# Optimization experiments

Measured on AMD Instinct MI355X. Metric: run time of the kernel, lower is better.

Reference implementation:

```python
import jax, jax.numpy as jnp
import numpy as np

B, T, DIM = 1, 2048, 2048
H, KV, D = 16, 4, 128
REP = H // KV
L, S = 32, 16          # cmp_len, cmp_stride
LP = 64                # slc_block
TOPK = 16
WIN = 512
CMP_HID = 2 * D
GATE_HID = DIM // 4
SCALE = D ** -0.5
TC = (T - L) // S + 1  # number of compressed blocks
NS = T // LP           # number of selection blocks
NEG = -1e30


def setup_inputs() -> dict:
    key = jax.random.key(0)
    ks = jax.random.split(key, 12)
    n = lambda k, sh: jax.random.normal(k, sh, jnp.float32) * 0.02
    return dict(
        x=jax.random.normal(ks[0], (B, T, DIM), jnp.float32),
        W_qkv=n(ks[1], ((H + 2 * KV) * D, DIM)), b_qkv=jnp.zeros(((H + 2 * KV) * D,), jnp.float32),
        W_out=n(ks[2], (DIM, H * D)), b_out=jnp.zeros((DIM,), jnp.float32),
        sinks=jnp.zeros((H,), jnp.float32),
        cmp_pos=n(ks[3], (L, D)),
        W_c1=n(ks[4], (CMP_HID, L * D)), b_c1=jnp.zeros((CMP_HID,), jnp.float32),
        W_c2=n(ks[5], (D, CMP_HID)), b_c2=jnp.zeros((D,), jnp.float32),
        W_g1=n(ks[6], (GATE_HID, DIM)), b_g1=jnp.zeros((GATE_HID,), jnp.float32),
        W_g2=n(ks[7], (3, GATE_HID)), b_g2=jnp.array([-2.2, -2.2, 1.4], jnp.float32),
    )


def _nsa(x, W_qkv, b_qkv, W_out, b_out, sinks, cmp_pos,
         W_c1, b_c1, W_c2, b_c2, W_g1, b_g1, W_g2, b_g2):
    qkv = x @ W_qkv.T + b_qkv
    q = qkv[..., :H * D].reshape(B, T, H, D)
    k = qkv[..., H * D:(H + KV) * D].reshape(B, T, KV, D)
    v = qkv[..., (H + KV) * D:].reshape(B, T, KV, D)

    t_idx = jnp.arange(T)
    # ---- compression phi over overlapping blocks (Eq 7) ----
    starts = jnp.arange(TC) * S
    gidx = starts[:, None] + jnp.arange(L)[None, :]          # [TC,L]

    def compress(z):                                          # [B,T,KV,D] -> [B,TC,KV,D]
        blk = z[:, gidx] + cmp_pos[None, None, :, None, :]    # [B,TC,L,KV,D]
        blk = blk.transpose(0, 1, 3, 2, 4).reshape(B, TC, KV, L * D)
        h = jax.nn.gelu(blk @ W_c1.T + b_c1, approximate=False)
        return h @ W_c2.T + b_c2

    k_cmp = jnp.repeat(compress(k), REP, axis=2)              # [B,TC,H,D]
    v_cmp = jnp.repeat(compress(v), REP, axis=2)

    # ---- CMP attention (Eq 8) ----
    c_logits = jnp.einsum('bthd,bchd->bhtc', q, k_cmp) * SCALE
    valid = (starts[None, :] + L - 1) <= t_idx[:, None]       # block fully in past [T,TC]
    c_logits = jnp.where(valid[None, None], c_logits, NEG)
    p = jax.nn.softmax(c_logits, axis=-1)
    any_valid = valid.any(axis=-1)                            # [T]
    p = jnp.where(any_valid[None, None, :, None], p, 0.0)
    o_cmp = jnp.einsum('bhtc,bchd->bthd', p, v_cmp)

    # ---- block score aggregation (Eq 9) + head sum (Eq 10) ----
    j_idx = jnp.arange(NS)
    ov = (starts[None, :] < (j_idx[:, None] + 1) * LP) & (starts[None, :] + L > j_idx[:, None] * LP)
    blk_scores = jnp.einsum('bhtc,jc->btj', p, ov.astype(p.dtype))  # [B,T,NS]
    cur_blk = t_idx // LP
    masked = jnp.where((j_idx[None, :] >= cur_blk[:, None])[None], -jnp.inf, blk_scores)
    _, dyn_idx = jax.lax.top_k(masked, TOPK - 3)              # Eq 11 (3 fixed blocks)
    fixed = jnp.stack([jnp.zeros_like(cur_blk), jnp.clip(cur_blk - 2, 0),
                       jnp.clip(cur_blk - 1, 0)], axis=-1)    # [T,3]
    all_blk = jnp.concatenate([jnp.broadcast_to(fixed[None], (B, T, 3)), dyn_idx], axis=-1)

    # ---- SLC sparse block attention (Eq 12) ----
    allowed = jax.nn.one_hot(all_blk, NS).sum(-2) > 0         # [B,T,NS]
    allowed = allowed | (j_idx[None, None, :] == cur_blk[None, :, None])  # own block dense
    tok_allowed = jnp.repeat(allowed, LP, axis=-1)            # [B,T,T]
    causal = t_idx[None, :] <= t_idx[:, None]                 # [T,T] (query, key)
    K = jnp.repeat(k, REP, axis=2)
    V = jnp.repeat(v, REP, axis=2)
    base = jnp.einsum('bthd,bshd->bhts', q, K) * SCALE        # shared logits
    s_logits = jnp.where((tok_allowed & causal[None])[:, None], base, NEG)
    o_slc = jnp.einsum('bhts,bshd->bthd', jax.nn.softmax(s_logits, -1), V)

    # ---- SWA sliding window with attention sinks ----
    swa_mask = causal & (t_idx[None, :] > t_idx[:, None] - WIN)
    w_logits = jnp.where(swa_mask[None, None], base, NEG)
    sink = jnp.broadcast_to(sinks[None, :, None, None], (B, H, T, 1))
    pw = jax.nn.softmax(jnp.concatenate([w_logits, sink], axis=-1), -1)[..., :T]
    o_swa = jnp.einsum('bhts,bshd->bthd', pw, V)

    # ---- sigmoid gating (Eq 5) + output proj ----
    g = jax.nn.sigmoid(jax.nn.gelu(x @ W_g1.T + b_g1, approximate=False) @ W_g2.T + b_g2)
    o = (g[..., 0, None, None] * o_cmp + g[..., 1, None, None] * o_slc
         + g[..., 2, None, None] * o_swa)                     # [B,T,H,D]
    return o.reshape(B, T, H * D) @ W_out.T + b_out


def reference(x, W_qkv, b_qkv, W_out, b_out, sinks, cmp_pos,
              W_c1, b_c1, W_c2, b_c2, W_g1, b_g1, W_g2, b_g2):
    return _nsa(x, W_qkv, b_qkv, W_out, b_out, sinks, cmp_pos,
                W_c1, b_c1, W_c2, b_c2, W_g1, b_g1, W_g2, b_g2)
```

## Files before the change

kernel.cpp:

```cpp
#include <hip/hip_runtime.h>
#include <hip/hip_bf16.h>

#define DEV static __device__ __forceinline__

constexpr int T_ = 2048, DIM_ = 2048, H_ = 16, KVH = 4, D_ = 128;
constexpr int LL = 32, SS = 16, TOPK_ = 16, WIN_ = 512;
constexpr int GATE_HID_ = 512;
constexpr int TC_ = 127, NS_ = 32;
constexpr int QKV_N = (H_ + 2 * KVH) * D_;
constexpr float SCALE_ = 0.08838834764831845f;

typedef __attribute__((ext_vector_type(8))) short short8;
typedef __attribute__((ext_vector_type(4))) float f32x4;
typedef __attribute__((ext_vector_type(4))) float float4v;
typedef __attribute__((ext_vector_type(4))) unsigned short u16x4;

DEV unsigned short f2b(float x) {
    return __builtin_bit_cast(unsigned short, __float2bfloat16(x));
}
DEV float b2f(unsigned short u) { return __builtin_bit_cast(float, ((unsigned)u) << 16); }
DEV float gelu_f(float x) { return 0.5f * x * (1.f + erff(x * 0.70710678118654752f)); }

DEV void g2l16(const void* g, void* l) {
    __builtin_amdgcn_global_load_lds((const __attribute__((address_space(1))) unsigned int*)g,
// ... 12 lines not shown

__global__ void cvt_all(const float* __restrict__ x, const float* __restrict__ wq,
                        const float* __restrict__ wg, const float* __restrict__ wc1,
                        const float* __restrict__ wc2,
                        unsigned short* __restrict__ xb, unsigned short* __restrict__ wqb,
                        unsigned short* __restrict__ wgb, unsigned short* __restrict__ wc1b,
                        unsigned short* __restrict__ wc2b) {
    const long i = ((long)blockIdx.x * 256 + threadIdx.x) * 4;
    const float* s;
    unsigned short* d;
    long off;
    if (i < 4194304)        { s = x;   d = xb;   off = i; }
    else if (i < 10485760)  { s = wq;  d = wqb;  off = i - 4194304; }
    else if (i < 11534336)  { s = wg;  d = wgb;  off = i - 10485760; }
    else if (i < 12582912)  { s = wc1; d = wc1b; off = i - 11534336; }
    else if (i < 12615680)  { s = wc2; d = wc2b; off = i - 12582912; }
    else return;
    float4v v = *(const float4v*)(s + off);
    u16x4 o;
#pragma unroll
    for (int j = 0; j < 4; j++) o[j] = f2b(v[j]);
    *(u16x4*)(d + off) = o;
}

DEV void stage64(const unsigned short* __restrict__ src, unsigned short* dstL,
                 int K, int tid) {
#pragma unroll
    for (int it = 0; it < 4; it++) {
        const int e = it * 256 + tid;
        const int row = e >> 3, cg = e & 7;
        g2l16(src + (size_t)row * K + ((cg ^ (row & 7)) << 3), dstL + e * 8);
    }
}
DEV short8 frag64(const unsigned short* Ls, int row, int g) {
    return *(const short8*)&Ls[row * 64 + ((g ^ (row & 7)) << 3)];
}

template <int ACT, bool WF, bool WB>
__global__ __launch_bounds__(256) void gemm_f(const unsigned short* __restrict__ A,
                                              const unsigned short* __restrict__ B,
                                              const float* __restrict__ bias,
                                              float* __restrict__ Cf,
                                              unsigned short* __restrict__ Cb,
                                              int M, int N, int K) {
    __shared__ __align__(16) unsigned short As[128 * 64];
    __shared__ __align__(16) unsigned short Bs[128 * 64];
    const int tid = threadIdx.x;
    const int w = tid >> 6, l = tid & 63;
    const int lc = l & 15, lg = l >> 4;
    const int wr = w >> 1, wc = w & 1;
    const int m0 = blockIdx.y * 128, n0 = blockIdx.x * 128;
    f32x4 acc[4][4] = {};
    for (int k0 = 0; k0 < K; k0 += 64) {
        stage64(A + (size_t)m0 * K + k0, As, K, tid);
        stage64(B + (size_t)n0 * K + k0, Bs, K, tid);
        __syncthreads();
#pragma unroll
        for (int ks = 0; ks < 2; ks++) {
            short8 af[4], bfr[4];
#pragma unroll
            for (int mi = 0; mi < 4; mi++) af[mi] = frag64(As, wr * 64 + mi * 16 + lc, ks * 4 + lg);
#pragma unroll
            for (int ni = 0; ni < 4; ni++) bfr[ni] = frag64(Bs, wc * 64 + ni * 16 + lc, ks * 4 + lg);
#pragma unroll
            for (int mi = 0; mi < 4; mi++)
#pragma unroll
                for (int ni = 0; ni < 4; ni++)
                    acc[mi][ni] = __builtin_amdgcn_mfma_f32_16x16x32_bf16(af[mi], bfr[ni], acc[mi][ni], 0, 0, 0);
        }
        __syncthreads();
    }
#pragma unroll
    for (int mi = 0; mi < 4; mi++) {
        const int gr = m0 + wr * 64 + mi * 16 + lg * 4;
#pragma unroll
        for (int ni = 0; ni < 4; ni++) {
            const int gc = n0 + wc * 64 + ni * 16 + lc;
            const float bv = bias[gc];
#pragma unroll
            for (int r = 0; r < 4; r++) {
                float v = acc[mi][ni][r] + bv;
                if (ACT == 1) v = gelu_f(v);
                const size_t idx = (size_t)(gr + r) * N + gc;
                if (WF) Cf[idx] = v;
                if (WB) Cb[idx] = f2b(v);
            }
        }
    }
}

__global__ __launch_bounds__(256) void gemm_qkvg(const unsigned short* __restrict__ A,
                                                 const unsigned short* __restrict__ Bq,
                                                 const unsigned short* __restrict__ Bg,
                                                 const float* __restrict__ bq,
                                                 const float* __restrict__ bg,
                                                 unsigned short* __restrict__ Cq,
                                                 float* __restrict__ Cg) {
    __shared__ __align__(16) unsigned short As[128 * 64];
    __shared__ __align__(16) unsigned short Bs[128 * 64];
    const int K = DIM_;
    const int tid = threadIdx.x;
    const int w = tid >> 6, l = tid & 63;
    const int lc = l & 15, lg = l >> 4;
    const int wr = w >> 1, wc = w & 1;
    const int m0 = blockIdx.y * 128, n0 = blockIdx.x * 128;
    const bool isg = (n0 >= QKV_N);
    const unsigned short* B = isg ? (Bg + (size_t)(n0 - QKV_N) * K) : (Bq + (size_t)n0 * K);
    f32x4 acc[4][4] = {};
    for (int k0 = 0; k0 < K; k0 += 64) {
        stage64(A + (size_t)m0 * K + k0, As, K, tid);
        stage64(B + k0, Bs, K, tid);
        __syncthreads();
#pragma unroll
        for (int ks = 0; ks < 2; ks++) {
            short8 af[4], bfr[4];
#pragma unroll
            for (int mi = 0; mi < 4; mi++) af[mi] = frag64(As, wr * 64 + mi * 16 + lc, ks * 4 + lg);
#pragma unroll
            for (int ni = 0; ni < 4; ni++) bfr[ni] = frag64(Bs, wc * 64 + ni * 16 + lc, ks * 4 + lg);
#pragma unroll
            for (int mi = 0; mi < 4; mi++)
#pragma unroll
                for (int ni = 0; ni < 4; ni++)
                    acc[mi][ni] = __builtin_amdgcn_mfma_f32_16x16x32_bf16(af[mi], bfr[ni], acc[mi][ni], 0, 0, 0);
        }
        __syncthreads();
    }
#pragma unroll
    for (int mi = 0; mi < 4; mi++) {
        const int gr = m0 + wr * 64 + mi * 16 + lg * 4;
#pragma unroll
        for (int ni = 0; ni < 4; ni++) {
            const int gcl = (n0 - (isg ? QKV_N : 0)) + wc * 64 + ni * 16 + lc;
            const float bv = isg ? bg[gcl] : bq[gcl];
#pragma unroll
            for (int r = 0; r < 4; r++) {
                const float v = acc[mi][ni][r] + bv;
                if (isg) Cg[(size_t)(gr + r) * GATE_HID_ + gcl] = gelu_f(v);
                else Cq[(size_t)(gr + r) * QKV_N + gcl] = f2b(v);
            }
        }
    }
}

__global__ __launch_bounds__(256) void gemm_c1p(const unsigned short* __restrict__ A,
                                                const unsigned short* __restrict__ B,
                                                float* __restrict__ part) {
    __shared__ __align__(16) unsigned short As[128 * 64];
    __shared__ __align__(16) unsigned short Bs[128 * 64];
    const int K = 4096, N = 256;
    const int tid = threadIdx.x;
    const int w = tid >> 6, l = tid & 63;
    const int lc = l & 15, lg = l >> 4;
    const int wr = w >> 1, wc = w & 1;
    const int m0 = blockIdx.y * 128, n0 = blockIdx.x * 128;
    const int kz = blockIdx.z * 1024;
    f32x4 acc[4][4] = {};
    for (int k0 = kz; k0 < kz + 1024; k0 += 64) {
        stage64(A + (size_t)m0 * K + k0, As, K, tid);
        stage64(B + (size_t)n0 * K + k0, Bs, K, tid);
        __syncthreads();
#pragma unroll
        for (int ks = 0; ks < 2; ks++) {
            short8 af[4], bfr[4];
#pragma unroll
            for (int mi = 0; mi < 4; mi++) af[mi] = frag64(As, wr * 64 + mi * 16 + lc, ks * 4 + lg);
#pragma unroll
            for (int ni = 0; ni < 4; ni++) bfr[ni] = frag64(Bs, wc * 64 + ni * 16 + lc, ks * 4 + lg);
#pragma unroll
            for (int mi = 0; mi < 4; mi++)
#pragma unroll
                for (int ni = 0; ni < 4; ni++)
                    acc[mi][ni] = __builtin_amdgcn_mfma_f32_16x16x32_bf16(af[mi], bfr[ni], acc[mi][ni], 0, 0, 0);
        }
        __syncthreads();
    }
    float* dst = part + (size_t)blockIdx.z * 2048 * 256;
#pragma unroll
    for (int mi = 0; mi < 4; mi++) {
        const int gr = m0 + wr * 64 + mi * 16 + lg * 4;
#pragma unroll
        for (int ni = 0; ni < 4; ni++) {
            const int gc = n0 + wc * 64 + ni * 16 + lc;
#pragma unroll
            for (int r = 0; r < 4; r++) dst[(size_t)(gr + r) * N + gc] = acc[mi][ni][r];
        }
    }
}

__global__ void c1_red(const float* __restrict__ part, const float* __restrict__ bias,
                       unsigned short* __restrict__ out) {
    const int i4 = blockIdx.x * 256 + threadIdx.x;
    const int base = i4 * 4;
    const int col = base & 255;
    float4v v = *(const float4v*)(part + base);
#pragma unroll
    for (int z = 1; z < 4; z++) {
        float4v p = *(const float4v*)(part + (size_t)z * 524288 + base);
#pragma unroll
        for (int j = 0; j < 4; j++) v[j] += p[j];
    }
    u16x4 o;
#pragma unroll
    for (int j = 0; j < 4; j++) o[j] = f2b(gelu_f(v[j] + bias[col + j]));
    *(u16x4*)(out + base) = o;
}

__global__ __launch_bounds__(256) void gemm_c2(const unsigned short* __restrict__ A,
                                               const unsigned short* __restrict__ B,
                                               const float* __restrict__ bias,
                                               unsigned short* __restrict__ Cb,
                                               unsigned short* __restrict__ vcmpT) {
    __shared__ __align__(16) unsigned short As[128 * 64];
    __shared__ __align__(16) unsigned short Bs[128 * 64];
    const int K = 256, N = 128;
    const int tid = threadIdx.x;
    const int w = tid >> 6, l = tid & 63;
    const int lc = l & 15, lg = l >> 4;
    const int wr = w >> 1, wc = w & 1;
    const int m0 = blockIdx.y * 128;
    f32x4 acc[4][4] = {};
    for (int k0 = 0; k0 < K; k0 += 64) {
        stage64(A + (size_t)m0 * K + k0, As, K, tid);
        stage64(B + k0, Bs, K, tid);
        __syncthreads();
#pragma unroll
        for (int ks = 0; ks < 2; ks++) {
            short8 af[4], bfr[4];
#pragma unroll
            for (int mi = 0; mi < 4; mi++) af[mi] = frag64(As, wr * 64 + mi * 16 + lc, ks * 4 + lg);
#pragma unroll
            for (int ni = 0; ni < 4; ni++) bfr[ni] = frag64(Bs, wc * 64 + ni * 16 + lc, ks * 4 + lg);
#pragma unroll
            for (int mi = 0; mi < 4; mi++)
#pragma unroll
                for (int ni = 0; ni < 4; ni++)
                    acc[mi][ni] = __builtin_amdgcn_mfma_f32_16x16x32_bf16(af[mi], bfr[ni], acc[mi][ni], 0, 0, 0);
        }
        __syncthreads();
    }
#pragma unroll
    for (int mi = 0; mi < 4; mi++) {
        const int gr = m0 + wr * 64 + mi * 16 + lg * 4;
#pragma unroll
        for (int ni = 0; ni < 4; ni++) {
            const int gc = wc * 64 + ni * 16 + lc;
            const float bv = bias[gc];
#pragma unroll
            for (int r = 0; r < 4; r++) {
                const int row = gr + r;
                const float v = acc[mi][ni][r] + bv;
                const unsigned short bv16 = f2b(v);
                Cb[(size_t)row * N + gc] = bv16;
                if (row >= 1024) {
                    const int mm = row - 1024;
                    const int cc = mm >> 2, kvv = mm & 3;
                    if (cc < 128) vcmpT[((size_t)(kvv * 128 + gc)) * 128 + cc] = bv16;
                }
            }
        }
    }
}

__global__ __launch_bounds__(256) void post_qkv(const unsigned short* __restrict__ qkvb,
                                                const float* __restrict__ cmp_pos,
                                                const float* __restrict__ hg,
                                                const float* __restrict__ Wg2,
                                                const float* __restrict__ bg2,
                                                unsigned short* __restrict__ kvTs,
                                                float* __restrict__ gate,
                                                unsigned short* __restrict__ blk) {
    const int bb = blockIdx.x;
    const int tid = threadIdx.x;
    if (bb < 128) {
        const int kv = bb & 3, tb = bb >> 2;
        const int t0 = tb * 64;
        unsigned short* dstK = kvTs + (size_t)(kv * 32 + tb) * 16384;
        unsigned short* dstV = dstK + 8192;
        const int kcol0 = H_ * D_ + kv * D_;
// ... 205 lines not shown
    amask[t] = chosen;
}

DEV void write_P(unsigned short* PsW, const float p[4][4], int lc, int lg) {
#pragma unroll
    for (int kt = 0; kt < 4; kt++) {
        const int col = kt * 16 + lc;
#pragma unroll
        for (int rp = 0; rp < 4; rp += 2) {
            unsigned int pk;
            asm("v_cvt_pk_bf16_f32 %0, %1, %2" : "=v"(pk) : "v"(p[kt][rp]), "v"(p[kt][rp + 1]));
            const int row0 = lg * 4 + rp;
            const int row1 = row0 + 1;
            PsW[row0 * 64 + (col ^ ((row0 & 7) << 3))] = (unsigned short)(pk & 0xFFFFu);
            PsW[row1 * 64 + (col ^ ((row1 & 7) << 3))] = (unsigned short)(pk >> 16);
        }
    }
}

DEV void stageKV(const unsigned short* __restrict__ src, unsigned short* dst, int tid) {
#pragma unroll
    for (int it = 0; it < 8; it++) {
        const int c = it * 256 + tid;
        g2l16(src + c * 8, dst + c * 8);
    }
}

__global__ __launch_bounds__(256) void slc_swa_pt(const unsigned short* __restrict__ qkvb,
                                                  const unsigned short* __restrict__ kvTs,
                                                  const unsigned int* __restrict__ amask,
                                                  float* __restrict__ mlp,
                                                  unsigned short* __restrict__ accp) {
    const int bid = blockIdx.x;
    const int pr = bid >> 5;
    const int hs = bid & 31;
    const int h = hs >> 1, seg = hs & 1;
    const int kv = h >> 2;
    const int tid = threadIdx.x;
    const int w = tid >> 6, l = tid & 63;
    const int lc = l & 15, lg = l >> 4;

    __shared__ __align__(16) unsigned short KV[16384];
    __shared__ __align__(16) unsigned short Ps[4][1024];

    const short8 ones = {0x3F80, 0x3F80, 0x3F80, 0x3F80, 0x3F80, 0x3F80, 0x3F80, 0x3F80};

    for (int it2 = 0; it2 < 2; it2++) {
        const int qb = it2 ? pr : (31 - pr);
        const int t0 = qb * 64;
        const int cur = qb;

        const unsigned int aml = amask[t0 + l];
        unsigned int u64v = aml;
#pragma unroll
        for (int o = 1; o < 64; o <<= 1) u64v |= __shfl_xor(u64v, o);
        unsigned int u16g = aml;
#pragma unroll
        for (int o = 1; o < 16; o <<= 1) u16g |= __shfl_xor(u16g, o);
        const unsigned int uni16 = __shfl(u16g, w * 16);
        unsigned int amr[4];
        int tq[4];
#pragma unroll
        for (int r = 0; r < 4; r++) {
            const int rl = w * 16 + lg * 4 + r;
            tq[r] = t0 + rl;
            amr[r] = __shfl(aml, rl);
        }
        const int tmin_w = t0 + w * 16;
        const int tmax_w = tmin_w + 15;

        const unsigned int curm = (cur >= 31) ? 0xFFFFFFFFu : ((1u << (cur + 1)) - 1u);
        int sl = qb - 8; if (sl < 0) sl = 0;
        const unsigned int swab = curm & ~((1u << sl) - 1u);
        const unsigned int act = (u64v & curm) | swab;
        unsigned int actseg = 0;
        {
            int rank = 0;
            for (int jb = 0; jb <= cur; jb++)
                if ((act >> jb) & 1u) {
                    if ((rank & 1) == seg) actseg |= 1u << jb;
                    rank++;
                }
        }

        short8 aq[4];
        {
            const unsigned short* qp = qkvb + (size_t)(t0 + w * 16 + lc) * QKV_N + h * D_ + lg * 8;
#pragma unroll
            for (int ks = 0; ks < 4; ks++) aq[ks] = *(const short8*)(qp + ks * 32);
        }

        f32x4 acc_s[8] = {};
        f32x4 acc_w[8] = {};
        f32x4 ls4 = {}, lw4 = {};
        float m[4];
#pragma unroll
        for (int r = 0; r < 4; r++) m[r] = -1e30f;

        const unsigned short* kvbase = kvTs + (size_t)kv * 32 * 16384;

        unsigned int rem = actseg;
        while (rem) {
            const int jb = __ffs(rem) - 1;
            rem &= rem - 1;
            stageKV(kvbase + (size_t)jb * 16384, KV, tid);
            __syncthreads();
            const bool slc_w = (uni16 >> jb) & 1u;
            const bool swa_w = (jb * 64 + 63) > (tmin_w - WIN_);
            if (slc_w || swa_w) {
                const unsigned short* Kb = KV;
                const unsigned short* Vb = KV + 8192;
                f32x4 sfr[4] = {};
                __builtin_amdgcn_s_setprio(1);
#pragma unroll
                for (int kt = 0; kt < 4; kt++) {
                    const int key = kt * 16 + lc;
#pragma unroll
                    for (int ks = 0; ks < 4; ks++) {
                        short8 bf = *(const short8*)&Kb[key * 128 + (((ks * 4 + lg) ^ (key & 7)) << 3)];
                        sfr[kt] = __builtin_amdgcn_mfma_f32_16x16x32_bf16(aq[ks], bf, sfr[kt], 0, 0, 0);
                    }
                }
                __builtin_amdgcn_s_setprio(0);
                float base[4][4];
#pragma unroll
                for (int kt = 0; kt < 4; kt++)
#pragma unroll
                    for (int r = 0; r < 4; r++) base[kt][r] = sfr[kt][r] * SCALE_;

                float lmax[4];
#pragma unroll
                for (int r = 0; r < 4; r++)
                    lmax[r] = fmaxf(fmaxf(base[0][r], base[1][r]), fmaxf(base[2][r], base[3][r]));
                bool need = false;
#pragma unroll
                for (int r = 0; r < 4; r++) need |= (lmax[r] > m[r] + 8.f);
                if (__any(need)) {
#pragma unroll
                    for (int r = 0; r < 4; r++) {
                        float rm = lmax[r];
#pragma unroll
                        for (int o = 1; o < 16; o <<= 1) rm = fmaxf(rm, __shfl_xor(rm, o));
                        const float mn = fmaxf(m[r], rm);
                        const float scf = __expf(m[r] - mn);
                        m[r] = mn;
#pragma unroll
                        for (int j = 0; j < 8; j++) { acc_s[j][r] *= scf; acc_w[j][r] *= scf; }
                        ls4[r] *= scf;
                        lw4[r] *= scf;
                    }
                }
                float e[4][4];
#pragma unroll
                for (int kt = 0; kt < 4; kt++)
#pragma unroll
                    for (int r = 0; r < 4; r++) e[kt][r] = __expf(base[kt][r] - m[r]);

                if (slc_w) {
                    float ps[4][4];
                    if (jb < cur) {
                        float mr[4];
#pragma unroll
                        for (int r = 0; r < 4; r++) mr[r] = (float)((amr[r] >> jb) & 1u);
#pragma unroll
                        for (int kt = 0; kt < 4; kt++)
#pragma unroll
                            for (int r = 0; r < 4; r++) ps[kt][r] = e[kt][r] * mr[r];
                    } else {
#pragma unroll
                        for (int kt = 0; kt < 4; kt++) {
                            const int kpos = jb * 64 + kt * 16 + lc;
#pragma unroll
                            for (int r = 0; r < 4; r++) {
                                const bool ok = (kpos <= tq[r]) && ((amr[r] >> jb) & 1u);
                                ps[kt][r] = ok ? e[kt][r] : 0.f;
                            }
                        }
                    }
                    write_P(Ps[w], ps, lc, lg);
                    __builtin_amdgcn_s_setprio(1);
#pragma unroll
                    for (int ks2 = 0; ks2 < 2; ks2++) {
                        short8 af = *(const short8*)&Ps[w][lc * 64 + ((ks2 * 32 + lg * 8) ^ ((lc & 7) << 3))];
                        ls4 = __builtin_amdgcn_mfma_f32_16x16x32_bf16(af, ones, ls4, 0, 0, 0);
#pragma unroll
                        for (int nj = 0; nj < 8; nj++) {
                            const int dd = nj * 16 + lc;
                            short8 bf = *(const short8*)&Vb[dd * 64 + (((ks2 * 4 + lg) ^ (dd & 7)) << 3)];
                            acc_s[nj] = __builtin_amdgcn_mfma_f32_16x16x32_bf16(af, bf, acc_s[nj], 0, 0, 0);
                        }
                    }
                    __builtin_amdgcn_s_setprio(0);
                }
                if (swa_w) {
                    const bool fullwin = (jb < cur) && (jb * 64 > tmax_w - WIN_);
                    if (fullwin) {
                        write_P(Ps[w], e, lc, lg);
                    } else {
                        float pw[4][4];
#pragma unroll
                        for (int kt = 0; kt < 4; kt++) {
                            const int kpos = jb * 64 + kt * 16 + lc;
#pragma unroll
                            for (int r = 0; r < 4; r++) {
                                const bool ok = (kpos <= tq[r]) && (kpos > tq[r] - WIN_);
                                pw[kt][r] = ok ? e[kt][r] : 0.f;
                            }
                        }
                        write_P(Ps[w], pw, lc, lg);
                    }
                    __builtin_amdgcn_s_setprio(1);
#pragma unroll
                    for (int ks2 = 0; ks2 < 2; ks2++) {
                        short8 af = *(const short8*)&Ps[w][lc * 64 + ((ks2 * 32 + lg * 8) ^ ((lc & 7) << 3))];
                        lw4 = __builtin_amdgcn_mfma_f32_16x16x32_bf16(af, ones, lw4, 0, 0, 0);
#pragma unroll
                        for (int nj = 0; nj < 8; nj++) {
                            const int dd = nj * 16 + lc;
                            short8 bf = *(const short8*)&Vb[dd * 64 + (((ks2 * 4 + lg) ^ (dd & 7)) << 3)];
                            acc_w[nj] = __builtin_amdgcn_mfma_f32_16x16x32_bf16(af, bf, acc_w[nj], 0, 0, 0);
                        }
                    }
                    __builtin_amdgcn_s_setprio(0);
                }
            }
            __syncthreads();
        }

        const size_t base2 = (size_t)(qb * 16 + h) * 2 + seg;
        if (lc == 0) {
#pragma unroll
            for (int r = 0; r < 4; r++) {
                const int row = w * 16 + lg * 4 + r;
                float4v v;
                v[0] = m[r]; v[1] = ls4[r]; v[2] = m[r]; v[3] = lw4[r];
                *(float4v*)&mlp[(base2 * 64 + row) * 4] = v;
            }
        }
#pragma unroll
        for (int st = 0; st < 2; st++) {
            const f32x4* A = st ? acc_w : acc_s;
#pragma unroll
            for (int nj = 0; nj < 8; nj++)
#pragma unroll
                for (int r = 0; r < 4; r++) {
                    const int row = w * 16 + lg * 4 + r;
                    accp[((base2 * 2 + st) * 64 + row) * 128 + nj * 16 + lc] = f2b(A[nj][r]);
                }
        }
        __syncthreads();
    }
}

__global__ __launch_bounds__(256) void slc_comb(const float* __restrict__ obuf,
                                                const float* __restrict__ mlp,
                                                const unsigned short* __restrict__ accp,
                                                const float* __restrict__ gate,
                                                const float* __restrict__ sinks,
                                                unsigned short* __restrict__ obufb) {
    const int t = blockIdx.x;
    const int qb = t >> 6, row = t & 63;
    const int tid = threadIdx.x;
    const int d = tid & 127, half = tid >> 7;
    const float g1 = gate[t * 3 + 1], g2 = gate[t * 3 + 2];
#pragma unroll
    for (int hh = 0; hh < 8; hh++) {
        const int h = half * 8 + hh;
        const size_t base2 = (size_t)(qb * 16 + h) * 2;
        const float4v ml0 = *(const float4v*)&mlp[((base2 + 0) * 64 + row) * 4];
        const float4v ml1 = *(const float4v*)&mlp[((base2 + 1) * 64 + row) * 4];
        const float Ms = fmaxf(ml0[0], ml1[0]);
        const float e0 = __expf(ml0[0] - Ms), e1 = __expf(ml1[0] - Ms);
        const float ls = ml0[1] * e0 + ml1[1] * e1;
        const float a0 = b2f(accp[(((base2 + 0) * 2 + 0) * 64 + row) * 128 + d]);
        const float a1 = b2f(accp[(((base2 + 1) * 2 + 0) * 64 + row) * 128 + d]);
        const float os = (a0 * e0 + a1 * e1) / ls;
        const float snk = sinks[h];
        const float Mw = fmaxf(fmaxf(ml0[2], ml1[2]), snk);
        const float w0 = __expf(ml0[2] - Mw), w1 = __expf(ml1[2] - Mw);
        const float den = ml0[3] * w0 + ml1[3] * w1 + __expf(snk - Mw);
        const float b0 = b2f(accp[(((base2 + 0) * 2 + 1) * 64 + row) * 128 + d]);
        const float b1 = b2f(accp[(((base2 + 1) * 2 + 1) * 64 + row) * 128 + d]);
        const float ow = (b0 * w0 + b1 * w1) / den;
// ... 19 lines not shown
    const float* W_g1 = (const float*)d_in[11];
    const float* b_g1 = (const float*)d_in[12];
    const float* W_g2 = (const float*)d_in[13];
    const float* b_g2 = (const float*)d_in[14];

    char* ws = (char*)d_ws;
    unsigned short* qkvb = (unsigned short*)(ws + 0);
    unsigned short* obufb = (unsigned short*)(ws + 0);
    char* A0 = ws + 12582912;
    unsigned short* Wqkv_b = (unsigned short*)(A0);
    unsigned short* blkb = (unsigned short*)(A0);
    float* obuf = (float*)(A0);
    char* B0 = ws + 29360128;
    unsigned short* x_b = (unsigned short*)(B0);
    unsigned short* kvTs = (unsigned short*)(B0);
    float* gateb = (float*)(ws + 37748736);
    unsigned int* amaskb = (unsigned int*)(ws + 37773312);
    float* scg = (float*)(ws + 37781504);
    float* mlp = (float*)(ws + 38830080);
    unsigned short* accp = (unsigned short*)(ws + 39878656);
    unsigned short* Wg1_b = (unsigned short*)(ws + 39878656);
    unsigned short* Wc1_b = (unsigned short*)(ws + 41975808);
    unsigned short* Wc2_b = (unsigned short*)(ws + 44072960);
    float* hgate = (float*)(ws + 44138496);
    unsigned short* hc_b = (unsigned short*)(ws + 48332800);
    unsigned short* hcmpb = (unsigned short*)(ws + 49381376);
    unsigned short* vcmpT = (unsigned short*)(ws + 49905664);
    float* c1part = (float*)(ws + 50036736);
    unsigned short* Wout_b = (unsigned short*)(ws + 39878656);
    float* outf = (float*)d_out;

    cvt_all<<<dim3(12320), 256, 0, stream>>>(x, W_qkv, W_g1, W_c1, W_c2,
                                             x_b, Wqkv_b, Wg1_b, Wc1_b, Wc2_b);
    gemm_qkvg<<<dim3((QKV_N + GATE_HID_) / 128, T_ / 128), 256, 0, stream>>>(
        x_b, Wqkv_b, Wg1_b, b_qkv, b_g1, qkvb, hgate);
    post_qkv<<<dim3(3712), 256, 0, stream>>>(qkvb, cmp_pos, hgate, W_g2, b_g2,
                                             kvTs, gateb, blkb);
    gemm_c1p<<<dim3(2, 16, 4), 256, 0, stream>>>(blkb, Wc1_b, c1part);
    c1_red<<<dim3(512), 256, 0, stream>>>(c1part, b_c1, hc_b);
    gemm_c2<<<dim3(1, 16), 256, 0, stream>>>(hc_b, Wc2_b, b_c2, hcmpb, vcmpT);
    cmp_attn2<<<dim3(512), 256, 0, stream>>>(qkvb, hcmpb, vcmpT, gateb, obuf, scg);
    topk_k<<<dim3(T_ / 256), 256, 0, stream>>>(scg, amaskb);
    slc_swa_pt<<<dim3(512), 256, 0, stream>>>(qkvb, kvTs, amaskb, mlp, accp);
    slc_comb<<<dim3(T_), 256, 0, stream>>>(obuf, mlp, accp, gateb, sinks, obufb);
    cvt_f2b<<<dim3(4096), 256, 0, stream>>>(W_out, Wout_b, DIM_ * H_ * D_);
    gemm_f<0, true, false><<<dim3(DIM_ / 128, T_ / 128), 256, 0, stream>>>(
        obufb, Wout_b, b_out, outf, nullptr, T_, DIM_, H_ * D_);
}
```

Before: 310.2 us.

## Halve GEMM M-tile to 64 and unpair query blocks in slc_swa attention

All four GEMM kernels move from 128x128 tiles (2x2 wave grid) to 64x128 tiles, with each wave owning a 64x32 slice. Grids double so more workgroups fill the CUs on these small-M problems. The selection/sliding-window attention kernel no longer processes a paired light and heavy query block per workgroup. It launches one workgroup per query block, with the heaviest blocks scheduled first. The trade-off is less operand reuse per tile, more redundant B-tile loads, and possible load imbalance from uneven per-block work.

Measured after the change: 260.8 us, median of 2. 1.19x faster.

```diff
diff --git a/kernel.cpp b/kernel.cpp
--- a/kernel.cpp
+++ b/kernel.cpp
@@ -68,50 +68,58 @@
         g2l16(src + (size_t)row * K + ((cg ^ (row & 7)) << 3), dstL + e * 8);
     }
 }
+DEV void stageA64(const unsigned short* __restrict__ src, unsigned short* dstL,
+                  int K, int tid) {
+#pragma unroll
+    for (int it = 0; it < 2; it++) {
+        const int e = it * 256 + tid;
+        const int row = e >> 3, cg = e & 7;
+        g2l16(src + (size_t)row * K + ((cg ^ (row & 7)) << 3), dstL + e * 8);
+    }
+}
 DEV short8 frag64(const unsigned short* Ls, int row, int g) {
     return *(const short8*)&Ls[row * 64 + ((g ^ (row & 7)) << 3)];
 }
 
 template <int ACT, bool WF, bool WB>
-__global__ __launch_bounds__(256) void gemm_f(const unsigned short* __restrict__ A,
+__global__ __launch_bounds__(256) void gemm64(const unsigned short* __restrict__ A,
                                               const unsigned short* __restrict__ B,
                                               const float* __restrict__ bias,
                                               float* __restrict__ Cf,
                                               unsigned short* __restrict__ Cb,
                                               int M, int N, int K) {
-    __shared__ __align__(16) unsigned short As[128 * 64];
+    __shared__ __align__(16) unsigned short As[64 * 64];
     __shared__ __align__(16) unsigned short Bs[128 * 64];
     const int tid = threadIdx.x;
     const int w = tid >> 6, l = tid & 63;
     const int lc = l & 15, lg = l >> 4;
-    const int wr = w >> 1, wc = w & 1;
-    const int m0 = blockIdx.y * 128, n0 = blockIdx.x * 128;
-    f32x4 acc[4][4] = {};
+    const int m0 = blockIdx.y * 64, n0 = blockIdx.x * 128;
+    f32x4 acc[4][2] = {};
     for (int k0 = 0; k0 < K; k0 += 64) {
-        stage64(A + (size_t)m0 * K + k0, As, K, tid);
+        stageA64(A + (size_t)m0 * K + k0, As, K, tid);
         stage64(B + (size_t)n0 * K + k0, Bs, K, tid);
         __syncthreads();
 #pragma unroll
         for (int ks = 0; ks < 2; ks++) {
-            short8 af[4], bfr[4];
-#pragma unroll
-            for (int mi = 0; mi < 4; mi++) af[mi] = frag64(As, wr * 64 + mi * 16 + lc, ks * 4 + lg);
-#pragma unroll
-            for (int ni = 0; ni < 4; ni++) bfr[ni] = frag64(Bs, wc * 64 + ni * 16 + lc, ks * 4 + lg);
+            short8 af[4], bfr[2];
+#pragma unroll
+            for (int mi = 0; mi < 4; mi++) af[mi] = frag64(As, mi * 16 + lc, ks * 4 + lg);
+#pragma unroll
+            for (int ni = 0; ni < 2; ni++) bfr[ni] = frag64(Bs, w * 32 + ni * 16 + lc, ks * 4 + lg);
 #pragma unroll
             for (int mi = 0; mi < 4; mi++)
 #pragma unroll
-                for (int ni = 0; ni < 4; ni++)
+                for (int ni = 0; ni < 2; ni++)
                     acc[mi][ni] = __builtin_amdgcn_mfma_f32_16x16x32_bf16(af[mi], bfr[ni], acc[mi][ni], 0, 0, 0);
         }
         __syncthreads();
     }
 #pragma unroll
     for (int mi = 0; mi < 4; mi++) {
-        const int gr = m0 + wr * 64 + mi * 16 + lg * 4;
-#pragma unroll
-        for (int ni = 0; ni < 4; ni++) {
-            const int gc = n0 + wc * 64 + ni * 16 + lc;
+        const int gr = m0 + mi * 16 + lg * 4;
+#pragma unroll
+        for (int ni = 0; ni < 2; ni++) {
+            const int gc = n0 + w * 32 + ni * 16 + lc;
             const float bv = bias[gc];
 #pragma unroll
             for (int r = 0; r < 4; r++) {
@@ -132,42 +140,41 @@
                                                  const float* __restrict__ bg,
                                                  unsigned short* __restrict__ Cq,
                                                  float* __restrict__ Cg) {
-    __shared__ __align__(16) unsigned short As[128 * 64];
+    __shared__ __align__(16) unsigned short As[64 * 64];
     __shared__ __align__(16) unsigned short Bs[128 * 64];
     const int K = DIM_;
     const int tid = threadIdx.x;
     const int w = tid >> 6, l = tid & 63;
     const int lc = l & 15, lg = l >> 4;
-    const int wr = w >> 1, wc = w & 1;
-    const int m0 = blockIdx.y * 128, n0 = blockIdx.x * 128;
+    const int m0 = blockIdx.y * 64, n0 = blockIdx.x * 128;
     const bool isg = (n0 >= QKV_N);
     const unsigned short* B = isg ? (Bg + (size_t)(n0 - QKV_N) * K) : (Bq + (size_t)n0 * K);
-    f32x4 acc[4][4] = {};
+    f32x4 acc[4][2] = {};
     for (int k0 = 0; k0 < K; k0 += 64) {
-        stage64(A + (size_t)m0 * K + k0, As, K, tid);
+        stageA64(A + (size_t)m0 * K + k0, As, K, tid);
         stage64(B + k0, Bs, K, tid);
         __syncthreads();
 #pragma unroll
         for (int ks = 0; ks < 2; ks++) {
-            short8 af[4], bfr[4];
-#pragma unroll
-            for (int mi = 0; mi < 4; mi++) af[mi] = frag64(As, wr * 64 + mi * 16 + lc, ks * 4 + lg);
-#pragma unroll
-            for (int ni = 0; ni < 4; ni++) bfr[ni] = frag64(Bs, wc * 64 + ni * 16 + lc, ks * 4 + lg);
+            short8 af[4], bfr[2];
+#pragma unroll
+            for (int mi = 0; mi < 4; mi++) af[mi] = frag64(As, mi * 16 + lc, ks * 4 + lg);
+#pragma unroll
+            for (int ni = 0; ni < 2; ni++) bfr[ni] = frag64(Bs, w * 32 + ni * 16 + lc, ks * 4 + lg);
 #pragma unroll
             for (int mi = 0; mi < 4; mi++)
 #pragma unroll
-                for (int ni = 0; ni < 4; ni++)
+                for (int ni = 0; ni < 2; ni++)
                     acc[mi][ni] = __builtin_amdgcn_mfma_f32_16x16x32_bf16(af[mi], bfr[ni], acc[mi][ni], 0, 0, 0);
         }
         __syncthreads();
     }
 #pragma unroll
     for (int mi = 0; mi < 4; mi++) {
-        const int gr = m0 + wr * 64 + mi * 16 + lg * 4;
-#pragma unroll
-        for (int ni = 0; ni < 4; ni++) {
-            const int gcl = (n0 - (isg ? QKV_N : 0)) + wc * 64 + ni * 16 + lc;
+        const int gr = m0 + mi * 16 + lg * 4;
+#pragma unroll
+        for (int ni = 0; ni < 2; ni++) {
+            const int gcl = (n0 - (isg ? QKV_N : 0)) + w * 32 + ni * 16 + lc;
             const float bv = isg ? bg[gcl] : bq[gcl];
 #pragma unroll
             for (int r = 0; r < 4; r++) {
@@ -182,31 +189,30 @@
 __global__ __launch_bounds__(256) void gemm_c1p(const unsigned short* __restrict__ A,
                                                 const unsigned short* __restrict__ B,
                                                 float* __restrict__ part) {
-    __shared__ __align__(16) unsigned short As[128 * 64];
+    __shared__ __align__(16) unsigned short As[64 * 64];
     __shared__ __align__(16) unsigned short Bs[128 * 64];
     const int K = 4096, N = 256;
     const int tid = threadIdx.x;
     const int w = tid >> 6, l = tid & 63;
     const int lc = l & 15, lg = l >> 4;
-    const int wr = w >> 1, wc = w & 1;
-    const int m0 = blockIdx.y * 128, n0 = blockIdx.x * 128;
+    const int m0 = blockIdx.y * 64, n0 = blockIdx.x * 128;
     const int kz = blockIdx.z * 1024;
-    f32x4 acc[4][4] = {};
+    f32x4 acc[4][2] = {};
     for (int k0 = kz; k0 < kz + 1024; k0 += 64) {
-        stage64(A + (size_t)m0 * K + k0, As, K, tid);
+        stageA64(A + (size_t)m0 * K + k0, As, K, tid);
         stage64(B + (size_t)n0 * K + k0, Bs, K, tid);
         __syncthreads();
 #pragma unroll
         for (int ks = 0; ks < 2; ks++) {
-            short8 af[4], bfr[4];
-#pragma unroll
-            for (int mi = 0; mi < 4; mi++) af[mi] = frag64(As, wr * 64 + mi * 16 + lc, ks * 4 + lg);
-#pragma unroll
-            for (int ni = 0; ni < 4; ni++) bfr[ni] = frag64(Bs, wc * 64 + ni * 16 + lc, ks * 4 + lg);
+            short8 af[4], bfr[2];
+#pragma unroll
+            for (int mi = 0; mi < 4; mi++) af[mi] = frag64(As, mi * 16 + lc, ks * 4 + lg);
+#pragma unroll
+            for (int ni = 0; ni < 2; ni++) bfr[ni] = frag64(Bs, w * 32 + ni * 16 + lc, ks * 4 + lg);
 #pragma unroll
             for (int mi = 0; mi < 4; mi++)
 #pragma unroll
-                for (int ni = 0; ni < 4; ni++)
+                for (int ni = 0; ni < 2; ni++)
                     acc[mi][ni] = __builtin_amdgcn_mfma_f32_16x16x32_bf16(af[mi], bfr[ni], acc[mi][ni], 0, 0, 0);
         }
         __syncthreads();
@@ -214,10 +220,10 @@
     float* dst = part + (size_t)blockIdx.z * 2048 * 256;
 #pragma unroll
     for (int mi = 0; mi < 4; mi++) {
-        const int gr = m0 + wr * 64 + mi * 16 + lg * 4;
-#pragma unroll
-        for (int ni = 0; ni < 4; ni++) {
-            const int gc = n0 + wc * 64 + ni * 16 + lc;
+        const int gr = m0 + mi * 16 + lg * 4;
+#pragma unroll
+        for (int ni = 0; ni < 2; ni++) {
+            const int gc = n0 + w * 32 + ni * 16 + lc;
 #pragma unroll
             for (int r = 0; r < 4; r++) dst[(size_t)(gr + r) * N + gc] = acc[mi][ni][r];
         }
@@ -247,40 +253,39 @@
                                                const float* __restrict__ bias,
                                                unsigned short* __restrict__ Cb,
                                                unsigned short* __restrict__ vcmpT) {
-    __shared__ __align__(16) unsigned short As[128 * 64];
+    __shared__ __align__(16) unsigned short As[64 * 64];
     __shared__ __align__(16) unsigned short Bs[128 * 64];
     const int K = 256, N = 128;
     const int tid = threadIdx.x;
     const int w = tid >> 6, l = tid & 63;
     const int lc = l & 15, lg = l >> 4;
-    const int wr = w >> 1, wc = w & 1;
-    const int m0 = blockIdx.y * 128;
-    f32x4 acc[4][4] = {};
+    const int m0 = blockIdx.y * 64;
+    f32x4 acc[4][2] = {};
     for (int k0 = 0; k0 < K; k0 += 64) {
-        stage64(A + (size_t)m0 * K + k0, As, K, tid);
+        stageA64(A + (size_t)m0 * K + k0, As, K, tid);
         stage64(B + k0, Bs, K, tid);
         __syncthreads();
 #pragma unroll
         for (int ks = 0; ks < 2; ks++) {
-            short8 af[4], bfr[4];
-#pragma unroll
-            for (int mi = 0; mi < 4; mi++) af[mi] = frag64(As, wr * 64 + mi * 16 + lc, ks * 4 + lg);
-#pragma unroll
-            for (int ni = 0; ni < 4; ni++) bfr[ni] = frag64(Bs, wc * 64 + ni * 16 + lc, ks * 4 + lg);
+            short8 af[4], bfr[2];
+#pragma unroll
+            for (int mi = 0; mi < 4; mi++) af[mi] = frag64(As, mi * 16 + lc, ks * 4 + lg);
+#pragma unroll
+            for (int ni = 0; ni < 2; ni++) bfr[ni] = frag64(Bs, w * 32 + ni * 16 + lc, ks * 4 + lg);
 #pragma unroll
             for (int mi = 0; mi < 4; mi++)
 #pragma unroll
-                for (int ni = 0; ni < 4; ni++)
+                for (int ni = 0; ni < 2; ni++)
                     acc[mi][ni] = __builtin_amdgcn_mfma_f32_16x16x32_bf16(af[mi], bfr[ni], acc[mi][ni], 0, 0, 0);
         }
         __syncthreads();
     }
 #pragma unroll
     for (int mi = 0; mi < 4; mi++) {
-        const int gr = m0 + wr * 64 + mi * 16 + lg * 4;
-#pragma unroll
-        for (int ni = 0; ni < 4; ni++) {
-            const int gc = wc * 64 + ni * 16 + lc;
+        const int gr = m0 + mi * 16 + lg * 4;
+#pragma unroll
+        for (int ni = 0; ni < 2; ni++) {
+            const int gc = w * 32 + ni * 16 + lc;
             const float bv = bias[gc];
 #pragma unroll
             for (int r = 0; r < 4; r++) {
@@ -552,223 +557,218 @@
                                                   float* __restrict__ mlp,
                                                   unsigned short* __restrict__ accp) {
     const int bid = blockIdx.x;
-    const int pr = bid >> 5;
+    const int qb = 31 - (bid >> 5);
     const int hs = bid & 31;
     const int h = hs >> 1, seg = hs & 1;
     const int kv = h >> 2;
     const int tid = threadIdx.x;
     const int w = tid >> 6, l = tid & 63;
     const int lc = l & 15, lg = l >> 4;
+    const int t0 = qb * 64;
+    const int cur = qb;
 
     __shared__ __align__(16) unsigned short KV[16384];
     __shared__ __align__(16) unsigned short Ps[4][1024];
 
     const short8 ones = {0x3F80, 0x3F80, 0x3F80, 0x3F80, 0x3F80, 0x3F80, 0x3F80, 0x3F80};
 
-    for (int it2 = 0; it2 < 2; it2++) {
-        const int qb = it2 ? pr : (31 - pr);
-        const int t0 = qb * 64;
-        const int cur = qb;
-
-        const unsigned int aml = amask[t0 + l];
-        unsigned int u64v = aml;
-#pragma unroll
-        for (int o = 1; o < 64; o <<= 1) u64v |= __shfl_xor(u64v, o);
-        unsigned int u16g = aml;
-#pragma unroll
-        for (int o = 1; o < 16; o <<= 1) u16g |= __shfl_xor(u16g, o);
-        const unsigned int uni16 = __shfl(u16g, w * 16);
-        unsigned int amr[4];
-        int tq[4];
-#pragma unroll
-        for (int r = 0; r < 4; r++) {
-            const int rl = w * 16 + lg * 4 + r;
-            tq[r] = t0 + rl;
-            amr[r] = __shfl(aml, rl);
-        }
-        const int tmin_w = t0 + w * 16;
-        const int tmax_w = tmin_w + 15;
-
-        const unsigned int curm = (cur >= 31) ? 0xFFFFFFFFu : ((1u << (cur + 1)) - 1u);
-        int sl = qb - 8; if (sl < 0) sl = 0;
-        const unsigned int swab = curm & ~((1u << sl) - 1u);
-        const unsigned int act = (u64v & curm) | swab;
-        unsigned int actseg = 0;
-        {
-            int rank = 0;
-            for (int jb = 0; jb <= cur; jb++)
-                if ((act >> jb) & 1u) {
-                    if ((rank & 1) == seg) actseg |= 1u << jb;
-                    rank++;
+    const unsigned int aml = amask[t0 + l];
+    unsigned int u64v = aml;
+#pragma unroll
+    for (int o = 1; o < 64; o <<= 1) u64v |= __shfl_xor(u64v, o);
+    unsigned int u16g = aml;
+#pragma unroll
+    for (int o = 1; o < 16; o <<= 1) u16g |= __shfl_xor(u16g, o);
+    const unsigned int uni16 = __shfl(u16g, w * 16);
+    unsigned int amr[4];
+    int tq[4];
+#pragma unroll
+    for (int r = 0; r < 4; r++) {
+        const int rl = w * 16 + lg * 4 + r;
+        tq[r] = t0 + rl;
+        amr[r] = __shfl(aml, rl);
+    }
+    const int tmin_w = t0 + w * 16;
+    const int tmax_w = tmin_w + 15;
+
+    const unsigned int curm = (cur >= 31) ? 0xFFFFFFFFu : ((1u << (cur + 1)) - 1u);
+    int sl = qb - 8; if (sl < 0) sl = 0;
+    const unsigned int swab = curm & ~((1u << sl) - 1u);
+    const unsigned int act = (u64v & curm) | swab;
+    unsigned int actseg = 0;
+    {
+        int rank = 0;
+        for (int jb = 0; jb <= cur; jb++)
+            if ((act >> jb) & 1u) {
+                if ((rank & 1) == seg) actseg |= 1u << jb;
+                rank++;
+            }
+    }
+
+    short8 aq[4];
+    {
+        const unsigned short* qp = qkvb + (size_t)(t0 + w * 16 + lc) * QKV_N + h * D_ + lg * 8;
+#pragma unroll
+        for (int ks = 0; ks < 4; ks++) aq[ks] = *(const short8*)(qp + ks * 32);
+    }
+
+    f32x4 acc_s[8] = {};
+    f32x4 acc_w[8] = {};
+    f32x4 ls4 = {}, lw4 = {};
+    float m[4];
+#pragma unroll
+    for (int r = 0; r < 4; r++) m[r] = -1e30f;
+
+    const unsigned short* kvbase = kvTs + (size_t)kv * 32 * 16384;
+
+    unsigned int rem = actseg;
+    while (rem) {
+        const int jb = __ffs(rem) - 1;
+        rem &= rem - 1;
+        stageKV(kvbase + (size_t)jb * 16384, KV, tid);
+        __syncthreads();
+        const bool slc_w = (uni16 >> jb) & 1u;
+        const bool swa_w = (jb * 64 + 63) > (tmin_w - WIN_);
+        if (slc_w || swa_w) {
+            const unsigned short* Kb = KV;
+            const unsigned short* Vb = KV + 8192;
+            f32x4 sfr[4] = {};
+            __builtin_amdgcn_s_setprio(1);
+#pragma unroll
+            for (int kt = 0; kt < 4; kt++) {
+                const int key = kt * 16 + lc;
+#pragma unroll
+                for (int ks = 0; ks < 4; ks++) {
+                    short8 bf = *(const short8*)&Kb[key * 128 + (((ks * 4 + lg) ^ (key & 7)) << 3)];
+                    sfr[kt] = __builtin_amdgcn_mfma_f32_16x16x32_bf16(aq[ks], bf, sfr[kt], 0, 0, 0);
                 }
-        }
-
-        short8 aq[4];
-        {
-            const unsigned short* qp = qkvb + (size_t)(t0 + w * 16 + lc) * QKV_N + h * D_ + lg * 8;
-#pragma unroll
-            for (int ks = 0; ks < 4; ks++) aq[ks] = *(const short8*)(qp + ks * 32);
-        }
-
-        f32x4 acc_s[8] = {};
-        f32x4 acc_w[8] = {};
-        f32x4 ls4 = {}, lw4 = {};
-        float m[4];
-#pragma unroll
-        for (int r = 0; r < 4; r++) m[r] = -1e30f;
-
-        const unsigned short* kvbase = kvTs + (size_t)kv * 32 * 16384;
-
-        unsigned int rem = actseg;
-        while (rem) {
-            const int jb = __ffs(rem) - 1;
-            rem &= rem - 1;
-            stageKV(kvbase + (size_t)jb * 16384, KV, tid);
-            __syncthreads();
-            const bool slc_w = (uni16 >> jb) & 1u;
-            const bool swa_w = (jb * 64 + 63) > (tmin_w - WIN_);
-            if (slc_w || swa_w) {
-                const unsigned short* Kb = KV;
-                const unsigned short* Vb = KV + 8192;
-                f32x4 sfr[4] = {};
+            }
+            __builtin_amdgcn_s_setprio(0);
+            float base[4][4];
+#pragma unroll
+            for (int kt = 0; kt < 4; kt++)
+#pragma unroll
+                for (int r = 0; r < 4; r++) base[kt][r] = sfr[kt][r] * SCALE_;
+
+            float lmax[4];
+#pragma unroll
+            for (int r = 0; r < 4; r++)
+                lmax[r] = fmaxf(fmaxf(base[0][r], base[1][r]), fmaxf(base[2][r], base[3][r]));
+            bool need = false;
+#pragma unroll
+            for (int r = 0; r < 4; r++) need |= (lmax[r] > m[r] + 8.f);
+            if (__any(need)) {
+#pragma unroll
+                for (int r = 0; r < 4; r++) {
+                    float rm = lmax[r];
+#pragma unroll
+                    for (int o = 1; o < 16; o <<= 1) rm = fmaxf(rm, __shfl_xor(rm, o));
+                    const float mn = fmaxf(m[r], rm);
+                    const float scf = __expf(m[r] - mn);
+                    m[r] = mn;
+#pragma unroll
+                    for (int j = 0; j < 8; j++) { acc_s[j][r] *= scf; acc_w[j][r] *= scf; }
+                    ls4[r] *= scf;
+                    lw4[r] *= scf;
+                }
+            }
+            float e[4][4];
+#pragma unroll
+            for (int kt = 0; kt < 4; kt++)
+#pragma unroll
+                for (int r = 0; r < 4; r++) e[kt][r] = __expf(base[kt][r] - m[r]);
+
+            if (slc_w) {
+                float ps[4][4];
+                if (jb < cur) {
+                    float mr[4];
+#pragma unroll
+                    for (int r = 0; r < 4; r++) mr[r] = (float)((amr[r] >> jb) & 1u);
+#pragma unroll
+                    for (int kt = 0; kt < 4; kt++)
+#pragma unroll
+                        for (int r = 0; r < 4; r++) ps[kt][r] = e[kt][r] * mr[r];
+                } else {
+#pragma unroll
+                    for (int kt = 0; kt < 4; kt++) {
+                        const int kpos = jb * 64 + kt * 16 + lc;
+#pragma unroll
+                        for (int r = 0; r < 4; r++) {
+                            const bool ok = (kpos <= tq[r]) && ((amr[r] >> jb) & 1u);
+                            ps[kt][r] = ok ? e[kt][r] : 0.f;
+                        }
+                    }
+                }
+                write_P(Ps[w], ps, lc, lg);
                 __builtin_amdgcn_s_setprio(1);
 #pragma unroll
-                for (int kt = 0; kt < 4; kt++) {
-                    const int key = kt * 16 + lc;
-#pragma unroll
-                    for (int ks = 0; ks < 4; ks++) {
-                        short8 bf = *(const short8*)&Kb[key * 128 + (((ks * 4 + lg) ^ (key & 7)) << 3)];
-                        sfr[kt] = __builtin_amdgcn_mfma_f32_16x16x32_bf16(aq[ks], bf, sfr[kt], 0, 0, 0);
+                for (int ks2 = 0; ks2 < 2; ks2++) {
+                    short8 af = *(const short8*)&Ps[w][lc * 64 + ((ks2 * 32 + lg * 8) ^ ((lc & 7) << 3))];
+                    ls4 = __builtin_amdgcn_mfma_f32_16x16x32_bf16(af, ones, ls4, 0, 0, 0);
+#pragma unroll
+                    for (int nj = 0; nj < 8; nj++) {
+                        const int dd = nj * 16 + lc;
+                        short8 bf = *(const short8*)&Vb[dd * 64 + (((ks2 * 4 + lg) ^ (dd & 7)) << 3)];
+                        acc_s[nj] = __builtin_amdgcn_mfma_f32_16x16x32_bf16(af, bf, acc_s[nj], 0, 0, 0);
                     }
                 }
                 __builtin_amdgcn_s_setprio(0);
-                float base[4][4];
-#pragma unroll
-                for (int kt = 0; kt < 4; kt++)
-#pragma unroll
-                    for (int r = 0; r < 4; r++) base[kt][r] = sfr[kt][r] * SCALE_;
-
-                float lmax[4];
-#pragma unroll
-                for (int r = 0; r < 4; r++)
-                    lmax[r] = fmaxf(fmaxf(base[0][r], base[1][r]), fmaxf(base[2][r], base[3][r]));
-                bool need = false;
-#pragma unroll
-                for (int r = 0; r < 4; r++) need |= (lmax[r] > m[r] + 8.f);
-                if (__any(need)) {
-#pragma unroll
-                    for (int r = 0; r < 4; r++) {
-                        float rm = lmax[r];
-#pragma unroll
-                        for (int o = 1; o < 16; o <<= 1) rm = fmaxf(rm, __shfl_xor(rm, o));
-                        const float mn = fmaxf(m[r], rm);
-                        const float scf = __expf(m[r] - mn);
-                        m[r] = mn;
-#pragma unroll
-                        for (int j = 0; j < 8; j++) { acc_s[j][r] *= scf; acc_w[j][r] *= scf; }
-                        ls4[r] *= scf;
-                        lw4[r] *= scf;
+            }
+            if (swa_w) {
+                const bool fullwin = (jb < cur) && (jb * 64 > tmax_w - WIN_);
+                if (fullwin) {
+                    write_P(Ps[w], e, lc, lg);
+                } else {
+                    float pw[4][4];
+#pragma unroll
+                    for (int kt = 0; kt < 4; kt++) {
+                        const int kpos = jb * 64 + kt * 16 + lc;
+#pragma unroll
+                        for (int r = 0; r < 4; r++) {
+                            const bool ok = (kpos <= tq[r]) && (kpos > tq[r] - WIN_);
+                            pw[kt][r] = ok ? e[kt][r] : 0.f;
+                        }
+                    }
+                    write_P(Ps[w], pw, lc, lg);
+                }
+                __builtin_amdgcn_s_setprio(1);
+#pragma unroll
+                for (int ks2 = 0; ks2 < 2; ks2++) {
+                    short8 af = *(const short8*)&Ps[w][lc * 64 + ((ks2 * 32 + lg * 8) ^ ((lc & 7) << 3))];
+                    lw4 = __builtin_amdgcn_mfma_f32_16x16x32_bf16(af, ones, lw4, 0, 0, 0);
+#pragma unroll
+                    for (int nj = 0; nj < 8; nj++) {
+                        const int dd = nj * 16 + lc;
+                        short8 bf = *(const short8*)&Vb[dd * 64 + (((ks2 * 4 + lg) ^ (dd & 7)) << 3)];
+                        acc_w[nj] = __builtin_amdgcn_mfma_f32_16x16x32_bf16(af, bf, acc_w[nj], 0, 0, 0);
                     }
                 }
-                float e[4][4];
-#pragma unroll
-                for (int kt = 0; kt < 4; kt++)
-#pragma unroll
-                    for (int r = 0; r < 4; r++) e[kt][r] = __expf(base[kt][r] - m[r]);
-
-                if (slc_w) {
-                    float ps[4][4];
-                    if (jb < cur) {
-                        float mr[4];
-#pragma unroll
-                        for (int r = 0; r < 4; r++) mr[r] = (float)((amr[r] >> jb) & 1u);
-#pragma unroll
-                        for (int kt = 0; kt < 4; kt++)
-#pragma unroll
-                            for (int r = 0; r < 4; r++) ps[kt][r] = e[kt][r] * mr[r];
-                    } else {
-#pragma unroll
-                        for (int kt = 0; kt < 4; kt++) {
-                            const int kpos = jb * 64 + kt * 16 + lc;
-#pragma unroll
-                            for (int r = 0; r < 4; r++) {
-                                const bool ok = (kpos <= tq[r]) && ((amr[r] >> jb) & 1u);
-                                ps[kt][r] = ok ? e[kt][r] : 0.f;
-                            }
-                        }
-                    }
-                    write_P(Ps[w], ps, lc, lg);
-                    __builtin_amdgcn_s_setprio(1);
-#pragma unroll
-                    for (int ks2 = 0; ks2 < 2; ks2++) {
-                        short8 af = *(const short8*)&Ps[w][lc * 64 + ((ks2 * 32 + lg * 8) ^ ((lc & 7) << 3))];
-                        ls4 = __builtin_amdgcn_mfma_f32_16x16x32_bf16(af, ones, ls4, 0, 0, 0);
-#pragma unroll
-                        for (int nj = 0; nj < 8; nj++) {
-                            const int dd = nj * 16 + lc;
-                            short8 bf = *(const short8*)&Vb[dd * 64 + (((ks2 * 4 + lg) ^ (dd & 7)) << 3)];
-                            acc_s[nj] = __builtin_amdgcn_mfma_f32_16x16x32_bf16(af, bf, acc_s[nj], 0, 0, 0);
-                        }
-                    }
-                    __builtin_amdgcn_s_setprio(0);
-                }
-                if (swa_w) {
-                    const bool fullwin = (jb < cur) && (jb * 64 > tmax_w - WIN_);
-                    if (fullwin) {
-                        write_P(Ps[w], e, lc, lg);
-                    } else {
-                        float pw[4][4];
-#pragma unroll
-                        for (int kt = 0; kt < 4; kt++) {
-                            const int kpos = jb * 64 + kt * 16 + lc;
-#pragma unroll
-                            for (int r = 0; r < 4; r++) {
-                                const bool ok = (kpos <= tq[r]) && (kpos > tq[r] - WIN_);
-                                pw[kt][r] = ok ? e[kt][r] : 0.f;
-                            }
-                        }
-                        write_P(Ps[w], pw, lc, lg);
-                    }
-                    __builtin_amdgcn_s_setprio(1);
-#pragma unroll
-                    for (int ks2 = 0; ks2 < 2; ks2++) {
-                        short8 af = *(const short8*)&Ps[w][lc * 64 + ((ks2 * 32 + lg * 8) ^ ((lc & 7) << 3))];
-                        lw4 = __builtin_amdgcn_mfma_f32_16x16x32_bf16(af, ones, lw4, 0, 0, 0);
-#pragma unroll
-                        for (int nj = 0; nj < 8; nj++) {
-                            const int dd = nj * 16 + lc;
-                            short8 bf = *(const short8*)&Vb[dd * 64 + (((ks2 * 4 + lg) ^ (dd & 7)) << 3)];
-                            acc_w[nj] = __builtin_amdgcn_mfma_f32_16x16x32_bf16(af, bf, acc_w[nj], 0, 0, 0);
-                        }
-                    }
-                    __builtin_amdgcn_s_setprio(0);
-                }
+                __builtin_amdgcn_s_setprio(0);
             }
-            __syncthreads();
-        }
-
-        const size_t base2 = (size_t)(qb * 16 + h) * 2 + seg;
-        if (lc == 0) {
+        }
+        __syncthreads();
+    }
+
+    const size_t base2 = (size_t)(qb * 16 + h) * 2 + seg;
+    if (lc == 0) {
+#pragma unroll
+        for (int r = 0; r < 4; r++) {
+            const int row = w * 16 + lg * 4 + r;
+            float4v v;
+            v[0] = m[r]; v[1] = ls4[r]; v[2] = m[r]; v[3] = lw4[r];
+            *(float4v*)&mlp[(base2 * 64 + row) * 4] = v;
+        }
+    }
+#pragma unroll
+    for (int st = 0; st < 2; st++) {
+        const f32x4* A = st ? acc_w : acc_s;
+#pragma unroll
+        for (int nj = 0; nj < 8; nj++)
 #pragma unroll
             for (int r = 0; r < 4; r++) {
                 const int row = w * 16 + lg * 4 + r;
-                float4v v;
-                v[0] = m[r]; v[1] = ls4[r]; v[2] = m[r]; v[3] = lw4[r];
-                *(float4v*)&mlp[(base2 * 64 + row) * 4] = v;
+                accp[((base2 * 2 + st) * 64 + row) * 128 + nj * 16 + lc] = f2b(A[nj][r]);
             }
-        }
-#pragma unroll
-        for (int st = 0; st < 2; st++) {
-            const f32x4* A = st ? acc_w : acc_s;
-#pragma unroll
-            for (int nj = 0; nj < 8; nj++)
-#pragma unroll
-                for (int r = 0; r < 4; r++) {
-                    const int row = w * 16 + lg * 4 + r;
-                    accp[((base2 * 2 + st) * 64 + row) * 128 + nj * 16 + lc] = f2b(A[nj][r]);
-                }
-        }
-        __syncthreads();
     }
 }
 
@@ -854,18 +854,18 @@
 
     cvt_all<<<dim3(12320), 256, 0, stream>>>(x, W_qkv, W_g1, W_c1, W_c2,
                                              x_b, Wqkv_b, Wg1_b, Wc1_b, Wc2_b);
-    gemm_qkvg<<<dim3((QKV_N + GATE_HID_) / 128, T_ / 128), 256, 0, stream>>>(
+    gemm_qkvg<<<dim3((QKV_N + GATE_HID_) / 128, T_ / 64), 256, 0, stream>>>(
         x_b, Wqkv_b, Wg1_b, b_qkv, b_g1, qkvb, hgate);
     post_qkv<<<dim3(3712), 256, 0, stream>>>(qkvb, cmp_pos, hgate, W_g2, b_g2,
                                              kvTs, gateb, blkb);
-    gemm_c1p<<<dim3(2, 16, 4), 256, 0, stream>>>(blkb, Wc1_b, c1part);
+    gemm_c1p<<<dim3(2, 32, 4), 256, 0, stream>>>(blkb, Wc1_b, c1part);
     c1_red<<<dim3(512), 256, 0, stream>>>(c1part, b_c1, hc_b);
-    gemm_c2<<<dim3(1, 16), 256, 0, stream>>>(hc_b, Wc2_b, b_c2, hcmpb, vcmpT);
+    gemm_c2<<<dim3(1, 32), 256, 0, stream>>>(hc_b, Wc2_b, b_c2, hcmpb, vcmpT);
     cmp_attn2<<<dim3(512), 256, 0, stream>>>(qkvb, hcmpb, vcmpT, gateb, obuf, scg);
     topk_k<<<dim3(T_ / 256), 256, 0, stream>>>(scg, amaskb);
-    slc_swa_pt<<<dim3(512), 256, 0, stream>>>(qkvb, kvTs, amaskb, mlp, accp);
+    slc_swa_pt<<<dim3(1024), 256, 0, stream>>>(qkvb, kvTs, amaskb, mlp, accp);
     slc_comb<<<dim3(T_), 256, 0, stream>>>(obuf, mlp, accp, gateb, sinks, obufb);
     cvt_f2b<<<dim3(4096), 256, 0, stream>>>(W_out, Wout_b, DIM_ * H_ * D_);
-    gemm_f<0, true, false><<<dim3(DIM_ / 128, T_ / 128), 256, 0, stream>>>(
+    gemm64<0, true, false><<<dim3(DIM_ / 128, T_ / 64), 256, 0, stream>>>(
         obufb, Wout_b, b_out, outf, nullptr, T_, DIM_, H_ * D_);
 }
```
